# Performance work log

Measured on AMD Instinct MI355X. Metric: run time of the kernel, lower is better.

Reference implementation:

```python
import jax, jax.numpy as jnp
import numpy as np

B = 16
C = 80
LEVELS = [(128, 128, 8), (64, 64, 16), (32, 32, 32), (16, 16, 64), (8, 8, 128)]
TOPN = 1000
MIN_SCORE = 0.05
NMS_THR = 0.6
MAX_OBJ = 100


def setup_inputs() -> dict:
    key = jax.random.key(0)
    inp = {}
    for l, (H, W, s) in enumerate(LEVELS):
        key, k1, k2, k3 = jax.random.split(key, 4)
        inp[f"cls{l}"] = jax.random.uniform(k1, (B, H, W, C), jnp.float32)
        inp[f"reg{l}"] = jax.random.uniform(k2, (B, H, W, 4), jnp.float32) * 128.0
        inp[f"ctr{l}"] = jax.random.uniform(k3, (B, H, W, 1), jnp.float32)
        xs = (jnp.arange(W, dtype=jnp.float32) + 0.5) * s
        ys = (jnp.arange(H, dtype=jnp.float32) + 0.5) * s
        gx, gy = jnp.meshgrid(xs, ys)  # [H, W]
        pos = jnp.stack([gx, gy], axis=-1)  # [H, W, 2]
        inp[f"pos{l}"] = jnp.broadcast_to(pos, (B, H, W, 2))
    return inp


def _nms_one(scores, classes, bboxes):
    # scores [N], classes int32 [N], bboxes float [N, 4] (already int-truncated values)
    s = jnp.where(scores > MIN_SCORE, scores, -jnp.inf)  # score-threshold mask
    top_s, top_i = jax.lax.top_k(s, TOPN)  # sort descending, keep topn
    top_c = jax.lax.stop_gradient(classes[top_i].astype(jnp.float32))
    top_b = bboxes[top_i]
    valid = top_s > MIN_SCORE
    wh = top_b[:, 2:4] - top_b[:, 0:2]
    areas = jnp.clip(wh[:, 0] * wh[:, 1], 0.0001)
    ar = jnp.arange(TOPN)

    def body(i, suppressed):
        active = valid[i] & (~suppressed[i])
        b = top_b[i]
        tl = jnp.maximum(b[0:2], top_b[:, 0:2])
        br = jnp.minimum(b[2:4], top_b[:, 2:4])
        owh = jnp.clip(br - tl, 0.0)
        inter = owh[:, 0] * owh[:, 1]
        union = jnp.clip(areas[i] + areas - inter, 0.0001)
        iou = inter / union
        return suppressed | (active & (ar > i) & (iou >= NMS_THR))

    suppressed = jax.lax.fori_loop(0, TOPN, body, jnp.zeros((TOPN,), bool))
    keep = valid & (~suppressed)
    rank = jnp.cumsum(keep.astype(jnp.int32)) - 1
    # scatter kept detections (in score order) into first MAX_OBJ slots; slot MAX_OBJ is a dump
    idx = jnp.where(keep & (rank < MAX_OBJ), rank, MAX_OBJ)
    out_s = jnp.full((MAX_OBJ + 1,), -1.0, jnp.float32).at[idx].set(jnp.where(keep, top_s, -1.0))[:MAX_OBJ]
    out_c = jnp.full((MAX_OBJ + 1,), -1.0, jnp.float32).at[idx].set(jnp.where(keep, top_c, -1.0))[:MAX_OBJ]
    out_b = jnp.zeros((MAX_OBJ + 1, 4), jnp.float32).at[idx].set(jnp.where(keep[:, None], top_b, 0.0))[:MAX_OBJ]
    return out_s, out_c, out_b


def _forward(cls_list, reg_list, ctr_list, pos_list):
    ss, cc, bb = [], [], []
    for c, r, t, p in zip(cls_list, reg_list, ctr_list, pos_list):
        b = c.shape[0]
        c = c.reshape(b, -1, c.shape[-1])   # [B, HW, 80]
        r = r.reshape(b, -1, 4)             # [B, HW, 4]
        t = t.reshape(b, -1)                # [B, HW]
        p = p.reshape(b, -1, 2)             # [B, HW, 2]
        sc = jnp.sqrt(jnp.max(c, axis=2) * t)
        cl = jnp.argmax(c, axis=2).astype(jnp.int32)
        bmin = p - r[:, :, 0:2]
        bmax = p + r[:, :, 2:4]
        # torch .int() truncates toward zero; values are used as floats afterward
        box = jax.lax.stop_gradient(jnp.trunc(jnp.concatenate([bmin, bmax], axis=2)))
        ss.append(sc); cc.append(cl); bb.append(box)
    scores = jnp.concatenate(ss, axis=1)
    classes = jnp.concatenate(cc, axis=1)
    boxes = jnp.concatenate(bb, axis=1)
    return jax.vmap(_nms_one)(scores, classes, boxes)


def reference(cls0, cls1, cls2, cls3, cls4, reg0, reg1, reg2, reg3, reg4,
              ctr0, ctr1, ctr2, ctr3, ctr4, pos0, pos1, pos2, pos3, pos4):
    return _forward([cls0, cls1, cls2, cls3, cls4],
                    [reg0, reg1, reg2, reg3, reg4],
                    [ctr0, ctr1, ctr2, ctr3, ctr4],
                    [pos0, pos1, pos2, pos3, pos4])
```

## Files before the change

kernel.cpp:

```cpp
#include <hip/hip_runtime.h>
#include <stdint.h>

typedef unsigned int u32;
typedef unsigned long long u64;

#define NTOT 21824
#define NBATCH 16
#define TOPN 1000
#define MAXOBJ 100
#define CAP 2048
#define CAPC 8192

__global__ void zero_kernel(u32* __restrict__ h) {
    int i = blockIdx.x * 1024 + threadIdx.x;
    if (i < NBATCH * 2048 + NBATCH * 32) h[i] = 0;
}

__global__ __launch_bounds__(256) void decode_kernel(
    const float* __restrict__ cls0, const float* __restrict__ cls1,
    const float* __restrict__ cls2, const float* __restrict__ cls3,
    const float* __restrict__ cls4,
    const float* __restrict__ reg0, const float* __restrict__ reg1,
    const float* __restrict__ reg2, const float* __restrict__ reg3,
    const float* __restrict__ reg4,
    const float* __restrict__ ctr0, const float* __restrict__ ctr1,
    const float* __restrict__ ctr2, const float* __restrict__ ctr3,
    const float* __restrict__ ctr4,
    u32* __restrict__ keys, int* __restrict__ clsidx, float4* __restrict__ boxes,
    u32* __restrict__ hist0)
{
    __shared__ u32 bh[2048];
    for (int i = threadIdx.x; i < 2048; i += 256) bh[i] = 0;
    __syncthreads();

    int loc = blockIdx.x * 256 + threadIdx.x;
    int b = blockIdx.y;
    if (loc < NTOT) {
        const float *cp, *rp, *tp;
        int li, wsh; float st;
        if (loc < 16384)      { li = loc;         wsh = 7; st = 8.f;   size_t o = (size_t)b*16384 + li; cp = cls0 + o*80; rp = reg0 + o*4; tp = ctr0 + o; }
        else if (loc < 20480) { li = loc - 16384; wsh = 6; st = 16.f;  size_t o = (size_t)b*4096  + li; cp = cls1 + o*80; rp = reg1 + o*4; tp = ctr1 + o; }
        else if (loc < 21504) { li = loc - 20480; wsh = 5; st = 32.f;  size_t o = (size_t)b*1024  + li; cp = cls2 + o*80; rp = reg2 + o*4; tp = ctr2 + o; }
        else if (loc < 21760) { li = loc - 21504; wsh = 4; st = 64.f;  size_t o = (size_t)b*256   + li; cp = cls3 + o*80; rp = reg3 + o*4; tp = ctr3 + o; }
        else                  { li = loc - 21760; wsh = 3; st = 128.f; size_t o = (size_t)b*64    + li; cp = cls4 + o*80; rp = reg4 + o*4; tp = ctr4 + o; }
        int wx = li & ((1 << wsh) - 1);
        int hy = li >> wsh;
        float px = ((float)wx + 0.5f) * st;
        float py = ((float)hy + 0.5f) * st;

        const float4* c4 = (const float4*)cp;
        float maxv = -1.0f; int arg = 0;
#pragma unroll
        for (int q = 0; q < 20; ++q) {
            float4 v = c4[q];
            if (v.x > maxv) { maxv = v.x; arg = 4*q;     }
            if (v.y > maxv) { maxv = v.y; arg = 4*q + 1; }
            if (v.z > maxv) { maxv = v.z; arg = 4*q + 2; }
            if (v.w > maxv) { maxv = v.w; arg = 4*q + 3; }
        }
        float ctr = *tp;
        float score = sqrtf(maxv * ctr);
        float4 r = *(const float4*)rp;
        float4 bx;
        bx.x = truncf(px - r.x); bx.y = truncf(py - r.y);
        bx.z = truncf(px + r.z); bx.w = truncf(py + r.w);
        size_t o = (size_t)b * NTOT + loc;
        u32 key = (score > 0.05f) ? (__float_as_uint(score) | 0x80000000u) : 0u;
        keys[o] = key;
        clsidx[o] = arg;
        boxes[o] = bx;
        if (key) atomicAdd(&bh[key >> 21], 1u);
    }
    __syncthreads();
    for (int i = threadIdx.x; i < 2048; i += 256) {
        u32 c = bh[i];
        if (c) atomicAdd(&hist0[b * 2048 + i], c);
    }
}

__global__ __launch_bounds__(1024) void pivot_kernel(
    const u32* __restrict__ keys, const u32* __restrict__ hist0,
    u32* __restrict__ params,
    float* __restrict__ tscore, float* __restrict__ tcls, float4* __restrict__ tbox)
{
    __shared__ u32 shist[2048];
    __shared__ u32 s_wtot[16];
    __shared__ int s_tf;
    __shared__ u32 s_C, s_above;
    int b = blockIdx.x, tid = threadIdx.x;
    int lane = tid & 63, wave = tid >> 6;
    const u32* kb = keys + (size_t)b * NTOT;

    for (int i = tid; i < TOPN; i += 1024) {
        size_t o = (size_t)b * TOPN + i;
        tscore[o] = -1.0f; tcls[o] = -1.0f;
        tbox[o] = make_float4(0.f, 0.f, 0.f, 0.f);
    }

    u32 h0 = hist0[b * 2048 + 2 * tid];
    u32 h1 = hist0[b * 2048 + 2 * tid + 1];
    if (tid == 0) s_tf = -1;
    u32 x = h0 + h1;
#pragma unroll
    for (int off = 1; off < 64; off <<= 1) {
        u32 y = __shfl_down(x, off);
        if (lane + off < 64) x += y;
    }
    if (lane == 0) s_wtot[wave] = x;
    __syncthreads();
    u32 wsuf = 0, tot = 0;
    for (int w2 = 0; w2 < 16; ++w2) { u32 v = s_wtot[w2]; tot += v; if (w2 > wave) wsuf += v; }
    u32 suf0 = x + wsuf, suf1 = suf0 - h0;
    u32 target = (tot < TOPN) ? tot : TOPN;

    if (target > 0) {
        if (suf0 >= target) atomicMax(&s_tf, 2 * tid);
        if (suf1 >= target) atomicMax(&s_tf, 2 * tid + 1);
    }
    __syncthreads();
    int t0 = s_tf;
    if (target > 0) {
        if (2 * tid == t0)     { s_C = suf0; s_above = suf0 - h0; }
        if (2 * tid + 1 == t0) { s_C = suf1; s_above = suf1 - h1; }
    }
    __syncthreads();
    u32 C0 = (target > 0) ? s_C : 0;
    u32 above0 = (target > 0) ? s_above : 0;

    bool need2 = (target > 0 && C0 > CAP);
    int t1 = 0; u32 C1 = 0, above1 = 0;
    shist[2 * tid] = 0; shist[2 * tid + 1] = 0;
    if (tid == 0) s_tf = -1;
    __syncthreads();
    if (need2) {
        for (int i = tid; i < NTOT; i += 1024) {
            u32 k = kb[i];
            if (k && (int)(k >> 21) == t0) atomicAdd(&shist[(k >> 10) & 2047], 1u);
        }
    }
    __syncthreads();
    {
        u32 g0 = shist[2 * tid], g1 = shist[2 * tid + 1];
        u32 x2 = g0 + g1;
#pragma unroll
        for (int off = 1; off < 64; off <<= 1) {
            u32 y = __shfl_down(x2, off);
            if (lane + off < 64) x2 += y;
        }
        if (lane == 0) s_wtot[wave] = x2;
        __syncthreads();
        u32 ws2 = 0;
        for (int w2 = wave + 1; w2 < 16; ++w2) ws2 += s_wtot[w2];
        u32 sa0 = x2 + ws2, sa1 = sa0 - g0;
        u32 need2c = target - above0;
        if (need2) {
            if (sa0 >= need2c) atomicMax(&s_tf, 2 * tid);
            if (sa1 >= need2c) atomicMax(&s_tf, 2 * tid + 1);
        }
        __syncthreads();
        t1 = s_tf;
        if (need2) {
            if (2 * tid == t1)     { s_C = above0 + sa0; s_above = above0 + sa0 - g0; }
            if (2 * tid + 1 == t1) { s_C = above0 + sa1; s_above = above0 + sa1 - g1; }
        }
        __syncthreads();
        if (need2) { C1 = s_C; above1 = s_above; }
    }

    bool need3 = (need2 && C1 > CAP);
    int t2 = 0;
    __syncthreads();
    shist[2 * tid] = 0; shist[2 * tid + 1] = 0;
    if (tid == 0) s_tf = -1;
    __syncthreads();
    if (need3) {
        for (int i = tid; i < NTOT; i += 1024) {
            u32 k = kb[i];
            if (k && (int)(k >> 21) == t0 && (int)((k >> 10) & 2047) == t1)
                atomicAdd(&shist[k & 1023], 1u);
        }
    }
    __syncthreads();
    {
        u32 g = shist[tid];
        u32 x3 = g;
#pragma unroll
        for (int off = 1; off < 64; off <<= 1) {
            u32 y = __shfl_down(x3, off);
            if (lane + off < 64) x3 += y;
        }
        if (lane == 0) s_wtot[wave] = x3;
        __syncthreads();
        u32 ws3 = 0;
        for (int w2 = wave + 1; w2 < 16; ++w2) ws3 += s_wtot[w2];
        u32 sb = x3 + ws3;
        if (need3) {
            u32 need3c = target - above1;
            if (sb >= need3c && tid < 1024) atomicMax(&s_tf, tid);
        }
        __syncthreads();
        t2 = s_tf;
    }

    if (tid == 0) {
        u32 P;
        if (target == 0)      P = 0xFFFFFFFFu;
        else if (!need2)      P = (u32)t0 << 21;
        else if (!need3)      P = ((u32)t0 << 21) | ((u32)t1 << 10);
        else                  P = ((u32)t0 << 21) | ((u32)t1 << 10) | (u32)t2;
        params[2 * b] = P;
        params[2 * b + 1] = target;
    }
}

__global__ __launch_bounds__(256) void gather_kernel(
    const u32* __restrict__ keys, const u32* __restrict__ params,
    u64* __restrict__ candbuf, u32* __restrict__ gcnt)
{
    __shared__ u32 s_wcnt[4];
    __shared__ u32 s_base;
    int b = blockIdx.y;
    int tid = threadIdx.x;
    int lane = tid & 63, wave = tid >> 6;
    u32 P = params[2 * b];
    int i = blockIdx.x * 256 + tid;
    u32 k = (i < NTOT) ? keys[(size_t)b * NTOT + i] : 0u;
    bool pass = (k != 0u) && (k >= P);
    u64 mask = __ballot(pass);
    if (lane == 0) s_wcnt[wave] = (u32)__popcll(mask);
    __syncthreads();
    if (tid == 0) {
        u32 tot = s_wcnt[0] + s_wcnt[1] + s_wcnt[2] + s_wcnt[3];
        s_base = tot ? atomicAdd(&gcnt[b * 32], tot) : 0u;
    }
    __syncthreads();
    if (pass) {
        u32 woff = 0;
        for (int w2 = 0; w2 < wave; ++w2) woff += s_wcnt[w2];
        u32 pos = s_base + woff + (u32)__popcll(mask & ((1ull << lane) - 1ull));
        if (pos < CAPC)
            candbuf[(size_t)b * CAPC + pos] = ((u64)k << 32) | (u32)(~i);
    }
}

__global__ __launch_bounds__(256) void rank_kernel(
    const u64* __restrict__ candbuf, const u32* __restrict__ gcnt,
    const u32* __restrict__ params,
    const int* __restrict__ clsidx, const float4* __restrict__ boxes,
    float* __restrict__ tscore, float* __restrict__ tcls, float4* __restrict__ tbox)
{
    int b = blockIdx.y;
    int lane = threadIdx.x & 63;
    u32 M = gcnt[b * 32]; if (M > CAPC) M = CAPC;
    u32 target = params[2 * b + 1];
    const u64* cb = candbuf + (size_t)b * CAPC;
    u32 Mr = (M + 63u) & ~63u;

    u32 wbase0 = blockIdx.x * 256 + (threadIdx.x & ~63u);
    for (u32 base = wbase0; base < M; base += 8 * 256) {
        u32 i0 = base + lane;
        bool val = (i0 < M);
        u64 e = val ? cb[i0] : ~0ull;
        u32 r = 0;
        for (u32 c0 = 0; c0 < Mr; c0 += 64) {
            u32 j = c0 + lane;
            u64 v = (j < M) ? cb[j] : 0ull;
            u32 vlo = (u32)v, vhi = (u32)(v >> 32);
#pragma unroll
            for (int s = 0; s < 64; ++s) {
                u32 lo = (u32)__builtin_amdgcn_readlane((int)vlo, s);
                u32 hi = (u32)__builtin_amdgcn_readlane((int)vhi, s);
                u64 vj = ((u64)hi << 32) | lo;
                r += (vj > e) ? 1u : 0u;
            }
        }
        if (val && r < target) {
            u32 k = (u32)(e >> 32);
            u32 loc = ~(u32)e;
            size_t src = (size_t)b * NTOT + loc;
            size_t o = (size_t)b * TOPN + r;
            tscore[o] = __uint_as_float(k & 0x7FFFFFFFu);
            tcls[o] = (float)clsidx[src];
            tbox[o] = boxes[src];
        }
    }
}

__global__ __launch_bounds__(256) void iou_kernel(
    const float4* __restrict__ tbox, u64* __restrict__ sup)
{
    __shared__ float4 sbox[TOPN];
    int b = blockIdx.y;
    int tid = threadIdx.x, lane = tid & 63, wave = tid >> 6;
    const float4* tb = tbox + (size_t)b * TOPN;
    for (int i = tid; i < TOPN; i += 256) sbox[i] = tb[i];
    __syncthreads();
    int i = blockIdx.x * 4 + wave;
    float4 bi = sbox[i];
    float areai = fmaxf((bi.z - bi.x) * (bi.w - bi.y), 0.0001f);
    u64* row = sup + ((size_t)b * TOPN + i) * 16;
#pragma unroll
    for (int w = 0; w < 16; ++w) {
        int col = w * 64 + lane;
        bool bit = false;
        if (col < TOPN) {
            float4 bj = sbox[col];
            float areaj = fmaxf((bj.z - bj.x) * (bj.w - bj.y), 0.0001f);
            float tlx = fmaxf(bi.x, bj.x), tly = fmaxf(bi.y, bj.y);
            float brx = fminf(bi.z, bj.z), bry = fminf(bi.w, bj.w);
            float ow = fmaxf(brx - tlx, 0.f), oh = fmaxf(bry - tly, 0.f);
            float inter = ow * oh;
            float uni = fmaxf(areai + areaj - inter, 0.0001f);
            bit = (col > i) && (inter / uni >= 0.6f);
        }
        u64 m = __ballot(bit);
        if (lane == 0) row[w] = m;
    }
}

#define CHROWS 128
#define NCHUNK 8

__global__ __launch_bounds__(1024) void finalize_kernel(
    const float* __restrict__ tscore, const float* __restrict__ tcls,
    const float4* __restrict__ tbox, const u64* __restrict__ sup,
    float* __restrict__ out)
{
    __shared__ u64 mat[2][CHROWS * 16];
    __shared__ u32 validsh[TOPN];
    __shared__ u64 removed_sh[16];
    __shared__ u32 wpref[17];
    int b = blockIdx.x, tid = threadIdx.x;
    int wave = tid >> 6, lane = tid & 63;

    for (int i = tid; i < TOPN; i += 1024)
        validsh[i] = (tscore[(size_t)b * TOPN + i] > 0.05f) ? 1u : 0u;

    const u64* supb = sup + (size_t)b * TOPN * 16;
    for (int idx = tid; idx < CHROWS * 16; idx += 1024)
        mat[0][idx] = supb[idx];
    __syncthreads();

    u64 my = 0;
    if (wave == 0) {
#pragma unroll
        for (int w2 = 0; w2 < 16; ++w2) {
            int i = w2 * 64 + lane;
            bool v = (i < TOPN) ? (validsh[i] != 0) : false;
            u64 m = __ballot(v);
            if (lane == w2) my = ~m;
        }
    }

    for (int chunk = 0; chunk < NCHUNK; ++chunk) {
        if (wave > 0 && chunk + 1 < NCHUNK) {
            int nr = (chunk + 1 == NCHUNK - 1) ? (TOPN - (NCHUNK - 1) * CHROWS) : CHROWS;
            const u64* src = supb + (size_t)(chunk + 1) * CHROWS * 16;
            u64* dst = mat[(chunk + 1) & 1];
            for (int idx = tid - 64; idx < nr * 16; idx += 960)
                dst[idx] = src[idx];
        }
        if (wave == 0) {
            int r0 = chunk * CHROWS;
            int rows = (chunk == NCHUNK - 1) ? (TOPN - r0) : CHROWS;
            int lw = lane & 15;
            const u64* M = mat[chunk & 1];
            for (int sub = 0; sub < rows; sub += 64) {
                int w2 = (r0 + sub) >> 6;
                u64 cur = __shfl(my, w2);
                int nsub = rows - sub; if (nsub > 64) nsub = 64;
                const u64* R = M + sub * 16;
                int ngrp = nsub >> 3;
                u64 cme[8], cww[8];
#pragma unroll
                for (int g = 0; g < 8; ++g) { cme[g] = R[g*16 + lw]; cww[g] = R[g*16 + w2]; }
                for (int grp = 0; grp < ngrp; ++grp) {
                    u64 nme[8] = {0,0,0,0,0,0,0,0}, nww[8] = {0,0,0,0,0,0,0,0};
                    if (grp + 1 < ngrp) {
                        const u64* Rn = R + (grp + 1) * 128;
#pragma unroll
                        for (int g = 0; g < 8; ++g) { nme[g] = Rn[g*16 + lw]; nww[g] = Rn[g*16 + w2]; }
                    }
#pragma unroll
                    for (int g = 0; g < 8; ++g) {
                        int u = grp * 8 + g;
                        u64 bit = (cur >> u) & 1ull;
                        u64 act = bit - 1ull;
                        cur |= cww[g] & act;
                        my  |= cme[g] & act;
                    }
#pragma unroll
                    for (int g = 0; g < 8; ++g) { cme[g] = nme[g]; cww[g] = nww[g]; }
                }
            }
        }
        __syncthreads();
    }
    if (wave == 0) {
        if (lane < 16) removed_sh[lane] = my;
        u32 pc = (lane < 16) ? (u32)__popcll(~my) : 0u;
#pragma unroll
        for (int off = 1; off < 16; off <<= 1) {
            u32 y = __shfl_up(pc, off);
            if (lane >= off) pc += y;
        }
        if (lane < 16) wpref[lane + 1] = pc;
        if (lane == 0) wpref[0] = 0;
    }
    __syncthreads();

    float* out_s = out;
    float* out_c = out + NBATCH * MAXOBJ;
    float* out_b = out + 2 * NBATCH * MAXOBJ;
    if (tid < MAXOBJ)     { out_s[b * MAXOBJ + tid] = -1.f; out_c[b * MAXOBJ + tid] = -1.f; }
    if (tid < MAXOBJ * 4) out_b[b * MAXOBJ * 4 + tid] = 0.f;
    __syncthreads();
    if (tid < TOPN) {
        u64 kw = ~removed_sh[tid >> 6];
        if ((kw >> (tid & 63)) & 1ull) {
            int rank = (int)wpref[tid >> 6] + (int)__popcll(kw & ((1ull << (tid & 63)) - 1ull));
            if (rank < MAXOBJ) {
                size_t o = (size_t)b * TOPN + tid;
                out_s[b * MAXOBJ + rank] = tscore[o];
                out_c[b * MAXOBJ + rank] = tcls[o];
                ((float4*)out_b)[b * MAXOBJ + rank] = tbox[o];
            }
        }
    }
}

extern "C" void kernel_launch(void* const* d_in, const int* in_sizes, int n_in,
                              void* d_out, int out_size, void* d_ws, size_t ws_size,
                              hipStream_t stream) {
    (void)in_sizes; (void)n_in; (void)out_size; (void)ws_size;
    const float* cls[5]; const float* reg[5]; const float* ctr[5];
    for (int l = 0; l < 5; ++l) {
        cls[l] = (const float*)d_in[4 * l + 0];
        reg[l] = (const float*)d_in[4 * l + 1];
        ctr[l] = (const float*)d_in[4 * l + 2];
    }
    char* w = (char*)d_ws;
    u32*    keys   = (u32*)(w + 0);
    int*    clsidx = (int*)(w + 1396736);
    float4* boxes  = (float4*)(w + 2793472);
    float*  tscore = (float*)(w + 8380416);
    float*  tcls   = (float*)(w + 8444416);
    float4* tbox   = (float4*)(w + 8508416);
    u64*    sup    = (u64*)(w + 8764416);
    u64*    candbuf= (u64*)(w + 8764416);
    u32*    hist0  = (u32*)(w + 9812992);
    u32*    gcnt   = (u32*)(w + 9944064);
    u32*    params = (u32*)(w + 9946112);

    zero_kernel<<<33, 1024, 0, stream>>>(hist0);
    decode_kernel<<<dim3((NTOT + 255) / 256, NBATCH), 256, 0, stream>>>(
        cls[0], cls[1], cls[2], cls[3], cls[4],
        reg[0], reg[1], reg[2], reg[3], reg[4],
        ctr[0], ctr[1], ctr[2], ctr[3], ctr[4],
        keys, clsidx, boxes, hist0);
    pivot_kernel<<<NBATCH, 1024, 0, stream>>>(keys, hist0, params, tscore, tcls, tbox);
    gather_kernel<<<dim3((NTOT + 255) / 256, NBATCH), 256, 0, stream>>>(keys, params, candbuf, gcnt);
    rank_kernel<<<dim3(8, NBATCH), 256, 0, stream>>>(candbuf, gcnt, params, clsidx, boxes,
                                                     tscore, tcls, tbox);
    iou_kernel<<<dim3(TOPN / 4, NBATCH), 256, 0, stream>>>(tbox, sup);
    finalize_kernel<<<NBATCH, 1024, 0, stream>>>(tscore, tcls, tbox, sup, (float*)d_out);
}
```

Measured before the change: 287.5 us.

## Split class argmax across 4 lanes and defer box decode to selected candidates

Decode now assigns four threads per location, each reading interleaved float4 chunks of the 80 class scores, then reduces max/argmax with xor shuffles (lowest index wins ties). Box regression decoding is removed from the full-grid pass and done in rank_kernel only for candidates that make the top-N. This aims to improve coalescing of the dominant class read and drop the full reg read and boxes write. It adds cross-lane shuffles and makes rank_kernel do scattered reg loads.

```diff
diff --git a/kernel.cpp b/kernel.cpp
--- a/kernel.cpp
+++ b/kernel.cpp
@@ -20,56 +20,53 @@
     const float* __restrict__ cls0, const float* __restrict__ cls1,
     const float* __restrict__ cls2, const float* __restrict__ cls3,
     const float* __restrict__ cls4,
-    const float* __restrict__ reg0, const float* __restrict__ reg1,
-    const float* __restrict__ reg2, const float* __restrict__ reg3,
-    const float* __restrict__ reg4,
     const float* __restrict__ ctr0, const float* __restrict__ ctr1,
     const float* __restrict__ ctr2, const float* __restrict__ ctr3,
     const float* __restrict__ ctr4,
-    u32* __restrict__ keys, int* __restrict__ clsidx, float4* __restrict__ boxes,
+    u32* __restrict__ keys, int* __restrict__ clsidx,
     u32* __restrict__ hist0)
 {
     __shared__ u32 bh[2048];
     for (int i = threadIdx.x; i < 2048; i += 256) bh[i] = 0;
     __syncthreads();
 
-    int loc = blockIdx.x * 256 + threadIdx.x;
+    int tid = threadIdx.x;
+    int g = tid >> 2, j = tid & 3;
+    int loc = blockIdx.x * 64 + g;
     int b = blockIdx.y;
     if (loc < NTOT) {
-        const float *cp, *rp, *tp;
-        int li, wsh; float st;
-        if (loc < 16384)      { li = loc;         wsh = 7; st = 8.f;   size_t o = (size_t)b*16384 + li; cp = cls0 + o*80; rp = reg0 + o*4; tp = ctr0 + o; }
-        else if (loc < 20480) { li = loc - 16384; wsh = 6; st = 16.f;  size_t o = (size_t)b*4096  + li; cp = cls1 + o*80; rp = reg1 + o*4; tp = ctr1 + o; }
-        else if (loc < 21504) { li = loc - 20480; wsh = 5; st = 32.f;  size_t o = (size_t)b*1024  + li; cp = cls2 + o*80; rp = reg2 + o*4; tp = ctr2 + o; }
-        else if (loc < 21760) { li = loc - 21504; wsh = 4; st = 64.f;  size_t o = (size_t)b*256   + li; cp = cls3 + o*80; rp = reg3 + o*4; tp = ctr3 + o; }
-        else                  { li = loc - 21760; wsh = 3; st = 128.f; size_t o = (size_t)b*64    + li; cp = cls4 + o*80; rp = reg4 + o*4; tp = ctr4 + o; }
-        int wx = li & ((1 << wsh) - 1);
-        int hy = li >> wsh;
-        float px = ((float)wx + 0.5f) * st;
-        float py = ((float)hy + 0.5f) * st;
+        const float *cp, *tp;
+        if (loc < 16384)      { size_t o = (size_t)b*16384 + loc;          cp = cls0 + o*80; tp = ctr0 + o; }
+        else if (loc < 20480) { size_t o = (size_t)b*4096  + (loc-16384);  cp = cls1 + o*80; tp = ctr1 + o; }
+        else if (loc < 21504) { size_t o = (size_t)b*1024  + (loc-20480);  cp = cls2 + o*80; tp = ctr2 + o; }
+        else if (loc < 21760) { size_t o = (size_t)b*256   + (loc-21504);  cp = cls3 + o*80; tp = ctr3 + o; }
+        else                  { size_t o = (size_t)b*64    + (loc-21760);  cp = cls4 + o*80; tp = ctr4 + o; }
 
         const float4* c4 = (const float4*)cp;
         float maxv = -1.0f; int arg = 0;
 #pragma unroll
-        for (int q = 0; q < 20; ++q) {
-            float4 v = c4[q];
-            if (v.x > maxv) { maxv = v.x; arg = 4*q;     }
-            if (v.y > maxv) { maxv = v.y; arg = 4*q + 1; }
-            if (v.z > maxv) { maxv = v.z; arg = 4*q + 2; }
-            if (v.w > maxv) { maxv = v.w; arg = 4*q + 3; }
-        }
-        float ctr = *tp;
-        float score = sqrtf(maxv * ctr);
-        float4 r = *(const float4*)rp;
-        float4 bx;
-        bx.x = truncf(px - r.x); bx.y = truncf(py - r.y);
-        bx.z = truncf(px + r.z); bx.w = truncf(py + r.w);
-        size_t o = (size_t)b * NTOT + loc;
-        u32 key = (score > 0.05f) ? (__float_as_uint(score) | 0x80000000u) : 0u;
-        keys[o] = key;
-        clsidx[o] = arg;
-        boxes[o] = bx;
-        if (key) atomicAdd(&bh[key >> 21], 1u);
+        for (int q = 0; q < 5; ++q) {
+            float4 v = c4[j + 4*q];
+            int ch = 16*q + 4*j;
+            if (v.x > maxv) { maxv = v.x; arg = ch;     }
+            if (v.y > maxv) { maxv = v.y; arg = ch + 1; }
+            if (v.z > maxv) { maxv = v.z; arg = ch + 2; }
+            if (v.w > maxv) { maxv = v.w; arg = ch + 3; }
+        }
+#pragma unroll
+        for (int d = 1; d <= 2; d <<= 1) {
+            float ov = __shfl_xor(maxv, d);
+            int   oa = __shfl_xor(arg, d);
+            if (ov > maxv || (ov == maxv && oa < arg)) { maxv = ov; arg = oa; }
+        }
+        if (j == 0) {
+            float score = sqrtf(maxv * (*tp));
+            u32 key = (score > 0.05f) ? (__float_as_uint(score) | 0x80000000u) : 0u;
+            size_t o = (size_t)b * NTOT + loc;
+            keys[o] = key;
+            clsidx[o] = arg;
+            if (key) atomicAdd(&bh[key >> 21], 1u);
+        }
     }
     __syncthreads();
     for (int i = threadIdx.x; i < 2048; i += 256) {
@@ -246,7 +243,10 @@
 __global__ __launch_bounds__(256) void rank_kernel(
     const u64* __restrict__ candbuf, const u32* __restrict__ gcnt,
     const u32* __restrict__ params,
-    const int* __restrict__ clsidx, const float4* __restrict__ boxes,
+    const int* __restrict__ clsidx,
+    const float* __restrict__ reg0, const float* __restrict__ reg1,
+    const float* __restrict__ reg2, const float* __restrict__ reg3,
+    const float* __restrict__ reg4,
     float* __restrict__ tscore, float* __restrict__ tcls, float4* __restrict__ tbox)
 {
     int b = blockIdx.y;
@@ -277,11 +277,25 @@
         if (val && r < target) {
             u32 k = (u32)(e >> 32);
             u32 loc = ~(u32)e;
+            const float* rp; float st; u32 li; int wsh;
+            if (loc < 16384u)      { li = loc;          wsh = 7; st = 8.f;   rp = reg0 + ((size_t)b*16384 + li)*4; }
+            else if (loc < 20480u) { li = loc - 16384u; wsh = 6; st = 16.f;  rp = reg1 + ((size_t)b*4096  + li)*4; }
+            else if (loc < 21504u) { li = loc - 20480u; wsh = 5; st = 32.f;  rp = reg2 + ((size_t)b*1024  + li)*4; }
+            else if (loc < 21760u) { li = loc - 21504u; wsh = 4; st = 64.f;  rp = reg3 + ((size_t)b*256   + li)*4; }
+            else                   { li = loc - 21760u; wsh = 3; st = 128.f; rp = reg4 + ((size_t)b*64    + li)*4; }
+            u32 wx = li & ((1u << wsh) - 1u);
+            u32 hy = li >> wsh;
+            float px = ((float)wx + 0.5f) * st;
+            float py = ((float)hy + 0.5f) * st;
+            float4 rg = *(const float4*)rp;
+            float4 bx;
+            bx.x = truncf(px - rg.x); bx.y = truncf(py - rg.y);
+            bx.z = truncf(px + rg.z); bx.w = truncf(py + rg.w);
             size_t src = (size_t)b * NTOT + loc;
             size_t o = (size_t)b * TOPN + r;
             tscore[o] = __uint_as_float(k & 0x7FFFFFFFu);
             tcls[o] = (float)clsidx[src];
-            tbox[o] = boxes[src];
+            tbox[o] = bx;
         }
     }
 }
@@ -442,7 +456,6 @@
     char* w = (char*)d_ws;
     u32*    keys   = (u32*)(w + 0);
     int*    clsidx = (int*)(w + 1396736);
-    float4* boxes  = (float4*)(w + 2793472);
     float*  tscore = (float*)(w + 8380416);
     float*  tcls   = (float*)(w + 8444416);
     float4* tbox   = (float4*)(w + 8508416);
@@ -453,14 +466,14 @@
     u32*    params = (u32*)(w + 9946112);
 
     zero_kernel<<<33, 1024, 0, stream>>>(hist0);
-    decode_kernel<<<dim3((NTOT + 255) / 256, NBATCH), 256, 0, stream>>>(
+    decode_kernel<<<dim3((NTOT + 63) / 64, NBATCH), 256, 0, stream>>>(
         cls[0], cls[1], cls[2], cls[3], cls[4],
-        reg[0], reg[1], reg[2], reg[3], reg[4],
         ctr[0], ctr[1], ctr[2], ctr[3], ctr[4],
-        keys, clsidx, boxes, hist0);
+        keys, clsidx, hist0);
     pivot_kernel<<<NBATCH, 1024, 0, stream>>>(keys, hist0, params, tscore, tcls, tbox);
     gather_kernel<<<dim3((NTOT + 255) / 256, NBATCH), 256, 0, stream>>>(keys, params, candbuf, gcnt);
-    rank_kernel<<<dim3(8, NBATCH), 256, 0, stream>>>(candbuf, gcnt, params, clsidx, boxes,
+    rank_kernel<<<dim3(8, NBATCH), 256, 0, stream>>>(candbuf, gcnt, params, clsidx,
+                                                     reg[0], reg[1], reg[2], reg[3], reg[4],
                                                      tscore, tcls, tbox);
     iou_kernel<<<dim3(TOPN / 4, NBATCH), 256, 0, stream>>>(tbox, sup);
     finalize_kernel<<<NBATCH, 1024, 0, stream>>>(tscore, tcls, tbox, sup, (float*)d_out);
```

Measured after the change: 278.0 us. 1.03x faster.
